# Kernel optimization log

Hardware: AMD Instinct MI355X
Metric: run time of the kernel (lower is better)

The kernel has to match this reference:

```python
import jax, jax.numpy as jnp
import numpy as np

TAU_THETA = 1.0   # membrane threshold V_th
GAMMA = 0.95      # spike reset decay factor
BETA = 0.95       # membrane leak factor

T, N = 128, 262144


def setup_inputs() -> dict:
    key = jax.random.key(0)
    I_in = jax.random.normal(key, (T, N), dtype=jnp.float32)
    return {"I_in": I_in}


def reference(I_in):
    # LIF recurrence over time via lax.scan (one fused sequential kernel).
    n = I_in.shape[1]
    v0 = jnp.zeros((n,), dtype=I_in.dtype)
    s0 = jnp.zeros((n,), dtype=I_in.dtype)

    def step(carry, I_t):
        v, s = carry
        v = BETA * v + I_t - GAMMA * s          # leak + input - reset current
        s = (v > TAU_THETA).astype(v.dtype)      # spike if above threshold
        v = v * (1.0 - s)                        # hard reset where spiked
        return (v, s), (s, v)

    _, (spikes, v_mem) = jax.lax.scan(step, (v0, s0), I_in)
    return (spikes, v_mem, spikes)
```

## Files before the change

kernel.cpp:

```cpp
#include <hip/hip_runtime.h>


#define T_STEPS 128
#define BETA_F 0.95f
#define GAMMA_F 0.95f
#define VTH_F 1.0f

typedef float f32x4 __attribute__((ext_vector_type(4)));

__global__ __launch_bounds__(256) void lif_kernel(
    const f32x4* __restrict__ I4,
    f32x4* __restrict__ s_out,
    f32x4* __restrict__ v_out,
    f32x4* __restrict__ s_out2,
    int n4)
{
    int idx = blockIdx.x * blockDim.x + threadIdx.x;
    if (idx >= n4) return;

    float vx = 0.f, vy = 0.f, vz = 0.f, vw = 0.f;
    float sx = 0.f, sy = 0.f, sz = 0.f, sw = 0.f;

    size_t off = (size_t)idx;
    #pragma unroll 8
    for (int t = 0; t < T_STEPS; ++t, off += (size_t)n4) {
        f32x4 in = I4[off];

        vx = __fsub_rn(__fadd_rn(__fmul_rn(BETA_F, vx), in.x), __fmul_rn(GAMMA_F, sx));
        vy = __fsub_rn(__fadd_rn(__fmul_rn(BETA_F, vy), in.y), __fmul_rn(GAMMA_F, sy));
        vz = __fsub_rn(__fadd_rn(__fmul_rn(BETA_F, vz), in.z), __fmul_rn(GAMMA_F, sz));
        vw = __fsub_rn(__fadd_rn(__fmul_rn(BETA_F, vw), in.w), __fmul_rn(GAMMA_F, sw));

        sx = (vx > VTH_F) ? 1.0f : 0.0f;
        sy = (vy > VTH_F) ? 1.0f : 0.0f;
        sz = (vz > VTH_F) ? 1.0f : 0.0f;
        sw = (vw > VTH_F) ? 1.0f : 0.0f;

        vx = (sx != 0.0f) ? 0.0f : vx;
        vy = (sy != 0.0f) ? 0.0f : vy;
        vz = (sz != 0.0f) ? 0.0f : vz;
        vw = (sw != 0.0f) ? 0.0f : vw;

        f32x4 sv; sv.x = sx; sv.y = sy; sv.z = sz; sv.w = sw;
        f32x4 vv; vv.x = vx; vv.y = vy; vv.z = vz; vv.w = vw;
        __builtin_nontemporal_store(sv, &s_out[off]);
        __builtin_nontemporal_store(vv, &v_out[off]);
        __builtin_nontemporal_store(sv, &s_out2[off]);
    }
}

extern "C" void kernel_launch(void* const* d_in, const int* in_sizes, int n_in,
                              void* d_out, int out_size, void* d_ws, size_t ws_size,
                              hipStream_t stream) {
    const float* I = (const float*)d_in[0];
    float* out = (float*)d_out;

    const int TN = in_sizes[0];
    const int N = TN / T_STEPS;
    const int n4 = N / 4;

    float* s0 = out;
    float* vm = out + (size_t)TN;
    float* s1 = out + 2 * (size_t)TN;

    const int block = 256;
    const int grid = (n4 + block - 1) / block;

    lif_kernel<<<grid, block, 0, stream>>>(
        (const f32x4*)I, (f32x4*)s0, (f32x4*)vm, (f32x4*)s1, n4);
}
```

Measured before the change: 75.59 us.

## Split time axis across two block groups with redundant prefix recomputation

Launches twice as many blocks, each handling half of the time steps for a column slice. The second-half blocks recompute the first half of the recurrence without storing anything, so they reach the correct state, then produce outputs for their own chunk. This doubles parallelism (256 blocks becomes 512 on a 256-CU device) and shortens each thread's serial dependency chain. The cost is about 50% more input reads and the redundant prefix compute.

```diff
diff --git a/kernel.cpp b/kernel.cpp
--- a/kernel.cpp
+++ b/kernel.cpp
@@ -2,11 +2,29 @@
 
 
 #define T_STEPS 128
+#define SPLIT 2
+#define T_CHUNK (T_STEPS / SPLIT)
 #define BETA_F 0.95f
 #define GAMMA_F 0.95f
 #define VTH_F 1.0f
 
 typedef float f32x4 __attribute__((ext_vector_type(4)));
+
+#define LIF_STEP(in)                                                            \
+    do {                                                                        \
+        vx = __fsub_rn(__fadd_rn(__fmul_rn(BETA_F, vx), (in).x), __fmul_rn(GAMMA_F, sx)); \
+        vy = __fsub_rn(__fadd_rn(__fmul_rn(BETA_F, vy), (in).y), __fmul_rn(GAMMA_F, sy)); \
+        vz = __fsub_rn(__fadd_rn(__fmul_rn(BETA_F, vz), (in).z), __fmul_rn(GAMMA_F, sz)); \
+        vw = __fsub_rn(__fadd_rn(__fmul_rn(BETA_F, vw), (in).w), __fmul_rn(GAMMA_F, sw)); \
+        sx = (vx > VTH_F) ? 1.0f : 0.0f;                                        \
+        sy = (vy > VTH_F) ? 1.0f : 0.0f;                                        \
+        sz = (vz > VTH_F) ? 1.0f : 0.0f;                                        \
+        sw = (vw > VTH_F) ? 1.0f : 0.0f;                                        \
+        vx = (sx != 0.0f) ? 0.0f : vx;                                          \
+        vy = (sy != 0.0f) ? 0.0f : vy;                                          \
+        vz = (sz != 0.0f) ? 0.0f : vz;                                          \
+        vw = (sw != 0.0f) ? 0.0f : vw;                                          \
+    } while (0)
 
 __global__ __launch_bounds__(256) void lif_kernel(
     const f32x4* __restrict__ I4,
@@ -15,32 +33,28 @@
     f32x4* __restrict__ s_out2,
     int n4)
 {
-    int idx = blockIdx.x * blockDim.x + threadIdx.x;
+    const int nblk = gridDim.x / SPLIT;
+    const int chunk = blockIdx.x / nblk;
+    const int bcol = blockIdx.x % nblk;
+    const int idx = bcol * blockDim.x + threadIdx.x;
     if (idx >= n4) return;
 
     float vx = 0.f, vy = 0.f, vz = 0.f, vw = 0.f;
     float sx = 0.f, sy = 0.f, sz = 0.f, sw = 0.f;
 
     size_t off = (size_t)idx;
+    const int t0 = chunk * T_CHUNK;
+
     #pragma unroll 8
-    for (int t = 0; t < T_STEPS; ++t, off += (size_t)n4) {
+    for (int t = 0; t < t0; ++t, off += (size_t)n4) {
         f32x4 in = I4[off];
+        LIF_STEP(in);
+    }
 
-        vx = __fsub_rn(__fadd_rn(__fmul_rn(BETA_F, vx), in.x), __fmul_rn(GAMMA_F, sx));
-        vy = __fsub_rn(__fadd_rn(__fmul_rn(BETA_F, vy), in.y), __fmul_rn(GAMMA_F, sy));
-        vz = __fsub_rn(__fadd_rn(__fmul_rn(BETA_F, vz), in.z), __fmul_rn(GAMMA_F, sz));
-        vw = __fsub_rn(__fadd_rn(__fmul_rn(BETA_F, vw), in.w), __fmul_rn(GAMMA_F, sw));
-
-        sx = (vx > VTH_F) ? 1.0f : 0.0f;
-        sy = (vy > VTH_F) ? 1.0f : 0.0f;
-        sz = (vz > VTH_F) ? 1.0f : 0.0f;
-        sw = (vw > VTH_F) ? 1.0f : 0.0f;
-
-        vx = (sx != 0.0f) ? 0.0f : vx;
-        vy = (sy != 0.0f) ? 0.0f : vy;
-        vz = (sz != 0.0f) ? 0.0f : vz;
-        vw = (sw != 0.0f) ? 0.0f : vw;
-
+    #pragma unroll 8
+    for (int t = 0; t < T_CHUNK; ++t, off += (size_t)n4) {
+        f32x4 in = I4[off];
+        LIF_STEP(in);
         f32x4 sv; sv.x = sx; sv.y = sy; sv.z = sz; sv.w = sw;
         f32x4 vv; vv.x = vx; vv.y = vy; vv.z = vz; vv.w = vw;
         __builtin_nontemporal_store(sv, &s_out[off]);
@@ -64,7 +78,8 @@
     float* s1 = out + 2 * (size_t)TN;
 
     const int block = 256;
-    const int grid = (n4 + block - 1) / block;
+    const int nblk = (n4 + block - 1) / block;
+    const int grid = nblk * SPLIT;
 
     lif_kernel<<<grid, block, 0, stream>>>(
         (const f32x4*)I, (f32x4*)s0, (f32x4*)vm, (f32x4*)s1, n4);
```

Result: slower. 80.53 us (+6.5%).
